# Performance work log

Hardware: AMD Instinct MI355X
Metric: run time of the kernel (lower is better)

The kernel has to match this reference:

```python
import jax, jax.numpy as jnp
import numpy as np


def setup_inputs() -> dict:
    key = jax.random.key(0)
    k1, k2, k3 = jax.random.split(key, 3)
    bs, n1, n2, d1, d2, dout = 4, 128, 128, 768, 768, 768
    input1 = jax.random.normal(k1, (bs, n1, d1), dtype=jnp.float32)
    input2 = jax.random.normal(k2, (bs, n2, d2), dtype=jnp.float32)
    # torch Linear(sum_dims, dout): we store W as (d1+d2, dout) so y = x @ W + b
    W = jax.random.normal(k3, (d1 + d2, dout), dtype=jnp.float32) * (1.0 / np.sqrt(d1 + d2))
    b = jnp.zeros((dout,), dtype=jnp.float32)
    return {"input1": input1, "input2": input2, "W": W, "b": b}


def reference(input1, input2, W, b):
    # Original: expand to [bs,n1,n2,d1]/[bs,n1,n2,d2], cat -> [bs,n1,n2,d1+d2], Linear.
    # Algebraically identical without materializing the concat:
    #   cat([x1,x2]) @ W = x1 @ W[:d1] + x2 @ W[d1:]
    d1 = input1.shape[-1]
    W1, W2 = W[:d1], W[d1:]
    p1 = jnp.einsum("bnd,do->bno", input1, W1)  # [bs, n1, dout]
    p2 = jnp.einsum("bmd,do->bmo", input2, W2)  # [bs, n2, dout]
    # broadcast-sum over the pair grid -> [bs, n1, n2, dout]
    return p1[:, :, None, :] + p2[:, None, :, :] + b
```

## Files before the change

kernel.cpp:

```cpp
#include <hip/hip_runtime.h>

typedef float f4 __attribute__((ext_vector_type(4)));

#define BK 16
#define TT 64
#define TO 64
#define NTILES 48

__global__ __launch_bounds__(512) void fused_kernel(
    const float* __restrict__ A1, const float* __restrict__ A2,
    const float* __restrict__ W, const float* __restrict__ bias,
    float* __restrict__ out)
{
    __shared__ union {
        float stage[2][4][BK][TT + 4];
        float pp[2][TT][TO + 4];
    } u;

    const int o0 = blockIdx.x * TO;
    const int nm = blockIdx.y;
    const int b  = nm >> 2;
    const int n0 = ((nm >> 1) & 1) * TT;
    const int m0 = (nm & 1) * TT;
    const int t  = threadIdx.x;
    const int h  = t >> 8;
    const int tl = t & 255;

    const int ln  = tl >> 2;
    const int lk4 = (tl & 3) * 4;
    const int wk  = tl >> 4;
    const int wo4 = (tl & 15) * 4;

    const float* Abase = h ? A2 : A1;
    const float* ap = Abase + (size_t)(b * 128 + (h ? m0 : n0) + ln) * 768 + lk4;
    const float* wp = W + (size_t)(h * 768 + wk) * 768 + o0 + wo4;

    const int tr = tl >> 4;
    const int tc = tl & 15;

    f4 av = *(const f4*)(ap);
    f4 wv = *(const f4*)(wp);
    #pragma unroll
    for (int i = 0; i < 4; ++i)
        u.stage[0][h][lk4 + i][ln] = av[i];
    *(f4*)&u.stage[0][2 + h][wk][wo4] = wv;
    __syncthreads();

    f4 acc[4] = {};
    int cur = 0;

    for (int tt = 0; tt < NTILES; ++tt) {
        if (tt + 1 < NTILES) {
            const int k0 = (tt + 1) * BK;
            av = *(const f4*)(ap + k0);
            wv = *(const f4*)(wp + (size_t)k0 * 768);
        }
        #pragma unroll
        for (int k = 0; k < BK; ++k) {
            const f4 x = *(const f4*)&u.stage[cur][h][k][tr * 4];
            const f4 y = *(const f4*)&u.stage[cur][2 + h][k][tc * 4];
            #pragma unroll
            for (int i = 0; i < 4; ++i)
                acc[i] += x[i] * y;
        }
        if (tt + 1 < NTILES) {
            const int nxt = cur ^ 1;
            #pragma unroll
            for (int i = 0; i < 4; ++i)
                u.stage[nxt][h][lk4 + i][ln] = av[i];
            *(f4*)&u.stage[nxt][2 + h][wk][wo4] = wv;
            __syncthreads();
        }
        cur ^= 1;
    }
    __syncthreads();

    #pragma unroll
    for (int i = 0; i < 4; ++i)
        *(f4*)&u.pp[h][tr * 4 + i][tc * 4] = acc[i];
    __syncthreads();

    const int o4 = (t & 15) * 4;
    const int nn = t >> 4;
    const f4 bb  = *(const f4*)(bias + o0 + o4);
    const f4 p1a = *(const f4*)&u.pp[0][nn * 2 + 0][o4] + bb;
    const f4 p1b = *(const f4*)&u.pp[0][nn * 2 + 1][o4] + bb;

    float* ob = out + ((size_t)(b * 128 + n0 + nn * 2) * 128 + m0) * 768 + o0 + o4;
    const size_t nstride = (size_t)128 * 768;

    #pragma unroll 4
    for (int m = 0; m < TT; ++m) {
        const f4 p2v = *(const f4*)&u.pp[1][m][o4];
        __builtin_nontemporal_store(p1a + p2v, (f4*)(ob + (size_t)m * 768));
        __builtin_nontemporal_store(p1b + p2v, (f4*)(ob + nstride + (size_t)m * 768));
    }
}

extern "C" void kernel_launch(void* const* d_in, const int* in_sizes, int n_in,
                              void* d_out, int out_size, void* d_ws, size_t ws_size,
                              hipStream_t stream)
{
    const float* input1 = (const float*)d_in[0];
    const float* input2 = (const float*)d_in[1];
    const float* W      = (const float*)d_in[2];
    const float* bias   = (const float*)d_in[3];
    float* out = (float*)d_out;

    fused_kernel<<<dim3(768 / TO, 16), 512, 0, stream>>>(input1, input2, W, bias, out);
}
```

Baseline: 296.0 us.

## Use bf16 MFMA with hi/lo split for the projection GEMMs

Replaces the scalar FP32 register-tiled GEMM with MFMA 16x16x32 bf16 instructions. Each FP32 operand is split into high and low bf16 parts, and three MFMAs are accumulated to approximate FP32 precision. Shared memory is relaid out into MFMA fragment order, and the K loop uses 32-wide chunks with register prefetch but a single LDS buffer. The gain from using matrix cores comes at the cost of conversion arithmetic, extra barriers, and slightly reduced precision.

New measurement: 268.3 us. -9.4%, faster.

```diff
diff --git a/kernel.cpp b/kernel.cpp
--- a/kernel.cpp
+++ b/kernel.cpp
@@ -1,11 +1,20 @@
 #include <hip/hip_runtime.h>
 
-typedef float f4 __attribute__((ext_vector_type(4)));
+typedef float f4    __attribute__((ext_vector_type(4)));
+typedef float f32x4 __attribute__((ext_vector_type(4)));
+typedef short short8 __attribute__((ext_vector_type(8)));
+typedef unsigned short u16x4 __attribute__((ext_vector_type(4)));
 
-#define BK 16
-#define TT 64
-#define TO 64
-#define NTILES 48
+#define NCHUNK 24
+
+__device__ inline unsigned short f2bf(float x) {
+    union { float f; unsigned u; } v; v.f = x;
+    return (unsigned short)((v.u + 0x7FFFu + ((v.u >> 16) & 1u)) >> 16);
+}
+__device__ inline float bf2f(unsigned short h) {
+    union { unsigned u; float f; } v; v.u = ((unsigned)h) << 16;
+    return v.f;
+}
 
 __global__ __launch_bounds__(512) void fused_kernel(
     const float* __restrict__ A1, const float* __restrict__ A2,
@@ -13,85 +22,125 @@
     float* __restrict__ out)
 {
     __shared__ union {
-        float stage[2][4][BK][TT + 4];
-        float pp[2][TT][TO + 4];
+        struct {
+            unsigned short Ah[4096], Al[4096], Bh[4096], Bl[4096];
+        } s;
+        float p[128][68];
     } u;
 
-    const int o0 = blockIdx.x * TO;
+    const int o0 = blockIdx.x * 64;
     const int nm = blockIdx.y;
     const int b  = nm >> 2;
-    const int n0 = ((nm >> 1) & 1) * TT;
-    const int m0 = (nm & 1) * TT;
-    const int t  = threadIdx.x;
-    const int h  = t >> 8;
-    const int tl = t & 255;
+    const int n0 = ((nm >> 1) & 1) * 64;
+    const int m0 = (nm & 1) * 64;
+    const int t    = threadIdx.x;
+    const int lane = t & 63;
+    const int w    = t >> 6;
 
-    const int ln  = tl >> 2;
-    const int lk4 = (tl & 3) * 4;
-    const int wk  = tl >> 4;
-    const int wo4 = (tl & 15) * 4;
+    const float* aptr[2]; int a_dst[2];
+    #pragma unroll
+    for (int q = 0; q < 2; ++q) {
+        const int a  = t + q * 512;
+        const int rc = a >> 3;
+        const int k0 = (a & 7) * 4;
+        const float* base = (rc < 64)
+            ? (A1 + (size_t)(b * 128 + n0 + rc) * 768)
+            : (A2 + (size_t)(b * 128 + m0 + (rc - 64)) * 768);
+        aptr[q]  = base + k0;
+        a_dst[q] = (rc >> 4) * 512 + (k0 >> 3) * 128 + (rc & 15) * 8 + (k0 & 7);
+    }
+    const float* bptr[2]; int b_dst[2];
+    #pragma unroll
+    for (int q = 0; q < 2; ++q) {
+        const int v  = t + q * 512;
+        const int oc = v & 127;
+        const int kk = (v >> 7) * 4;
+        const int z  = oc >> 6;
+        bptr[q]  = W + (size_t)(z * 768 + kk) * 768 + (o0 + (oc & 63));
+        b_dst[q] = (oc >> 4) * 512 + (kk >> 3) * 128 + (oc & 15) * 8 + (kk & 7);
+    }
 
-    const float* Abase = h ? A2 : A1;
-    const float* ap = Abase + (size_t)(b * 128 + (h ? m0 : n0) + ln) * 768 + lk4;
-    const float* wp = W + (size_t)(h * 768 + wk) * 768 + o0 + wo4;
+    f4 rA[2]; float rB[2][4];
+    #pragma unroll
+    for (int q = 0; q < 2; ++q) {
+        rA[q] = *(const f4*)(aptr[q]);
+        #pragma unroll
+        for (int j = 0; j < 4; ++j) rB[q][j] = bptr[q][(size_t)j * 768];
+    }
 
-    const int tr = tl >> 4;
-    const int tc = tl & 15;
+    f32x4 acc[4] = {0, 0, 0, 0};
 
-    f4 av = *(const f4*)(ap);
-    f4 wv = *(const f4*)(wp);
-    #pragma unroll
-    for (int i = 0; i < 4; ++i)
-        u.stage[0][h][lk4 + i][ln] = av[i];
-    *(f4*)&u.stage[0][2 + h][wk][wo4] = wv;
-    __syncthreads();
-
-    f4 acc[4] = {};
-    int cur = 0;
-
-    for (int tt = 0; tt < NTILES; ++tt) {
-        if (tt + 1 < NTILES) {
-            const int k0 = (tt + 1) * BK;
-            av = *(const f4*)(ap + k0);
-            wv = *(const f4*)(wp + (size_t)k0 * 768);
+    for (int c = 0; c < NCHUNK; ++c) {
+        #pragma unroll
+        for (int q = 0; q < 2; ++q) {
+            u16x4 h, l;
+            #pragma unroll
+            for (int j = 0; j < 4; ++j) {
+                h[j] = f2bf(rA[q][j]);
+                l[j] = f2bf(rA[q][j] - bf2f(h[j]));
+            }
+            *(u16x4*)&u.s.Ah[a_dst[q]] = h;
+            *(u16x4*)&u.s.Al[a_dst[q]] = l;
         }
         #pragma unroll
-        for (int k = 0; k < BK; ++k) {
-            const f4 x = *(const f4*)&u.stage[cur][h][k][tr * 4];
-            const f4 y = *(const f4*)&u.stage[cur][2 + h][k][tc * 4];
+        for (int q = 0; q < 2; ++q) {
+            u16x4 h, l;
             #pragma unroll
-            for (int i = 0; i < 4; ++i)
-                acc[i] += x[i] * y;
+            for (int j = 0; j < 4; ++j) {
+                h[j] = f2bf(rB[q][j]);
+                l[j] = f2bf(rB[q][j] - bf2f(h[j]));
+            }
+            *(u16x4*)&u.s.Bh[b_dst[q]] = h;
+            *(u16x4*)&u.s.Bl[b_dst[q]] = l;
         }
-        if (tt + 1 < NTILES) {
-            const int nxt = cur ^ 1;
+        __syncthreads();
+
+        if (c + 1 < NCHUNK) {
+            const int k0 = (c + 1) * 32;
             #pragma unroll
-            for (int i = 0; i < 4; ++i)
-                u.stage[nxt][h][lk4 + i][ln] = av[i];
-            *(f4*)&u.stage[nxt][2 + h][wk][wo4] = wv;
-            __syncthreads();
+            for (int q = 0; q < 2; ++q) {
+                rA[q] = *(const f4*)(aptr[q] + k0);
+                #pragma unroll
+                for (int j = 0; j < 4; ++j)
+                    rB[q][j] = bptr[q][(size_t)(k0 + j) * 768];
+            }
         }
-        cur ^= 1;
+
+        {
+            const short8 ah = *(const short8*)&u.s.Ah[w * 512 + lane * 8];
+            const short8 al = *(const short8*)&u.s.Al[w * 512 + lane * 8];
+            const int bt0 = (w >> 2) * 4;
+            #pragma unroll
+            for (int ct = 0; ct < 4; ++ct) {
+                const short8 bh = *(const short8*)&u.s.Bh[(bt0 + ct) * 512 + lane * 8];
+                const short8 bl = *(const short8*)&u.s.Bl[(bt0 + ct) * 512 + lane * 8];
+                acc[ct] = __builtin_amdgcn_mfma_f32_16x16x32_bf16(ah, bh, acc[ct], 0, 0, 0);
+                acc[ct] = __builtin_amdgcn_mfma_f32_16x16x32_bf16(ah, bl, acc[ct], 0, 0, 0);
+                acc[ct] = __builtin_amdgcn_mfma_f32_16x16x32_bf16(al, bh, acc[ct], 0, 0, 0);
+            }
+        }
+        __syncthreads();
     }
-    __syncthreads();
 
     #pragma unroll
-    for (int i = 0; i < 4; ++i)
-        *(f4*)&u.pp[h][tr * 4 + i][tc * 4] = acc[i];
+    for (int ct = 0; ct < 4; ++ct)
+        #pragma unroll
+        for (int i = 0; i < 4; ++i)
+            u.p[w * 16 + (lane >> 4) * 4 + i][ct * 16 + (lane & 15)] = acc[ct][i];
     __syncthreads();
 
     const int o4 = (t & 15) * 4;
     const int nn = t >> 4;
     const f4 bb  = *(const f4*)(bias + o0 + o4);
-    const f4 p1a = *(const f4*)&u.pp[0][nn * 2 + 0][o4] + bb;
-    const f4 p1b = *(const f4*)&u.pp[0][nn * 2 + 1][o4] + bb;
+    const f4 p1a = *(const f4*)&u.p[nn * 2 + 0][o4] + bb;
+    const f4 p1b = *(const f4*)&u.p[nn * 2 + 1][o4] + bb;
 
     float* ob = out + ((size_t)(b * 128 + n0 + nn * 2) * 128 + m0) * 768 + o0 + o4;
     const size_t nstride = (size_t)128 * 768;
 
     #pragma unroll 4
-    for (int m = 0; m < TT; ++m) {
-        const f4 p2v = *(const f4*)&u.pp[1][m][o4];
+    for (int m = 0; m < 64; ++m) {
+        const f4 p2v = *(const f4*)&u.p[64 + m][o4];
         __builtin_nontemporal_store(p1a + p2v, (f4*)(ob + (size_t)m * 768));
         __builtin_nontemporal_store(p1b + p2v, (f4*)(ob + nstride + (size_t)m * 768));
     }
@@ -107,5 +156,5 @@
     const float* bias   = (const float*)d_in[3];
     float* out = (float*)d_out;
 
-    fused_kernel<<<dim3(768 / TO, 16), 512, 0, stream>>>(input1, input2, W, bias, out);
+    fused_kernel<<<dim3(12, 16), 512, 0, stream>>>(input1, input2, W, bias, out);
 }
```
